# Kernel tuning notes

Measured on AMD Instinct MI355X. Metric: run time of the kernel, lower is better.

Reference implementation:

```python
import jax, jax.numpy as jnp
import numpy as np
import math

IN_FEATURES = 4096
OUT_FEATURES = 4096
NUM_COMPONENTS = 256
TWO_PI = 2.0 * math.pi


def setup_inputs() -> dict:
    key = jax.random.key(0)
    k1, k2, k3, k4 = jax.random.split(key, 4)
    x = jax.random.normal(k1, (4096, IN_FEATURES), dtype=jnp.float32)
    mus = jax.random.uniform(k2, (NUM_COMPONENTS, 2), dtype=jnp.float32)
    log_vars = -3.0 - jax.random.uniform(k3, (NUM_COMPONENTS, 2), dtype=jnp.float32)
    weights = jax.random.uniform(k4, (NUM_COMPONENTS,), dtype=jnp.float32) / NUM_COMPONENTS
    return {"x": x, "mus": mus, "log_vars": log_vars, "weights": weights}


def reference(x, mus, log_vars, weights):
    in_features = x.shape[1]
    x_in_idx = jnp.linspace(0.0, 1.0, in_features, dtype=jnp.float32)    # [I]
    x_out_idx = jnp.linspace(0.0, 1.0, OUT_FEATURES, dtype=jnp.float32)  # [O]
    vars_ = jnp.exp(log_vars)  # [M, 2]

    # Input-side Gaussian basis, fused with 1/sqrt(2*pi*var) and component weight: [I, M]
    d_in = (x_in_idx[:, None] - mus[None, :, 0]) ** 2
    G_in = jnp.exp(-d_in / (2.0 * vars_[None, :, 0])) / jnp.sqrt(TWO_PI * vars_[None, :, 0]) * weights[None, :]
    C = x @ G_in  # [B, M]

    # Output-side Gaussian pdf (Normal(mu1, sigma1).log_prob(x_out).exp()): [M, O]
    d_out = (x_out_idx[None, :] - mus[:, 1:2]) ** 2
    G_out = jnp.exp(-d_out / (2.0 * vars_[:, 1:2])) / jnp.sqrt(TWO_PI * vars_[:, 1:2])

    x_out = (C @ G_out) / (in_features * jnp.sum(weights))  # [B, O]
    return x_out
```

## Files before the change

### kernel.cpp

```cpp
#include <hip/hip_runtime.h>
#include <hip/hip_bf16.h>
#include <math.h>

#define IN_FEAT 4096
#define OUT_FEAT 4096
#define NCOMP 256
#define BATCH 4096
#define TWO_PI_F 6.28318530717958647692f

typedef __attribute__((ext_vector_type(8))) short short8;
typedef __attribute__((ext_vector_type(8))) __bf16 bf16x8;
typedef __attribute__((ext_vector_type(4))) float f32x4;
typedef __attribute__((ext_vector_type(16))) float f32x16;

__device__ __forceinline__ ushort f2b(float f) {
  union { float f; unsigned u; } v; v.f = f;
  unsigned r = (v.u + 0x7fffu + ((v.u >> 16) & 1u)) >> 16;
  return (ushort)r;
}

__device__ __forceinline__ float b2f(short s) {
  union { unsigned u; float f; } v; v.u = ((unsigned)(ushort)s) << 16;
  return v.f;
}

__device__ __forceinline__ bf16x8 ld_frag(const void* p) {
  short8 s = *(const short8*)p;
  return __builtin_bit_cast(bf16x8, s);
}

__device__ __forceinline__ bf16x8 cvt8f(float4 a, float4 b) {
  bf16x8 r;
  r[0] = (__bf16)a.x; r[1] = (__bf16)a.y; r[2] = (__bf16)a.z; r[3] = (__bf16)a.w;
  r[4] = (__bf16)b.x; r[5] = (__bf16)b.y; r[6] = (__bf16)b.z; r[7] = (__bf16)b.w;
  return r;
}

__device__ __forceinline__ void gload_lds16(const void* g, void* l) {
  __builtin_amdgcn_global_load_lds(
      (const __attribute__((address_space(1))) void*)g,
      (__attribute__((address_space(3))) void*)l, 16, 0, 0);
}

__global__ __launch_bounds__(256) void prep_kernel(
    const float* __restrict__ mus, const float* __restrict__ lvs,
    const float* __restrict__ w,
    ushort* __restrict__ Gt, ushort* __restrict__ GoT) {
  int idx = blockIdx.x * 256 + threadIdx.x;
  if (idx < NCOMP * IN_FEAT) {
    int m = idx >> 12, i = idx & (IN_FEAT - 1);
    float v = expf(lvs[2 * m]);
    float d = (float)i * (1.0f / (IN_FEAT - 1)) - mus[2 * m];
    float g = expf(-d * d * (0.5f / v)) * rsqrtf(TWO_PI_F * v) * w[m];
    Gt[idx] = f2b(g);
  } else {
    idx -= NCOMP * IN_FEAT;
    int o = idx >> 8, m = idx & (NCOMP - 1);
    float v = expf(lvs[2 * m + 1]);
    float d = (float)o * (1.0f / (OUT_FEAT - 1)) - mus[2 * m + 1];
    float g = expf(-d * d * (0.5f / v)) * rsqrtf(TWO_PI_F * v);
    GoT[idx] = f2b(g);
  }
}

template<int NS>
__global__ __launch_bounds__(256, 2) void gemm1_kernel(
    const float* __restrict__ x, const ushort* __restrict__ Gt,
    ushort* __restrict__ Cpart) {
  constexpr int KR = IN_FEAT / NS;
  constexpr int NT = KR / 32;
  __shared__ __align__(16) char lds[3 * 24576];
  const int tid = threadIdx.x, wid = tid >> 6, lane = tid & 63;
  const int m0 = blockIdx.x * 128;
  const int n0 = blockIdx.y * 128;
  const int kb0 = blockIdx.z * KR;
  const int l15 = lane & 15, q = lane >> 4;
  const int wr = (wid >> 1) * 64, wc = (wid & 1) * 64;

  f32x4 acc[4][4] = {};

  const int ar = lane >> 3;
  const int aslot = (lane & 7) ^ ar;
  const float* gpa[4];
  #pragma unroll
  for (int i = 0; i < 4; ++i) {
    int c = wid * 4 + i;
    gpa[i] = &x[(size_t)(m0 + c * 8 + ar) * IN_FEAT + kb0 + aslot * 4];
  }
  const int br = lane >> 2;
  const int bsw = (((lane & 3) ^ ((lane >> 3) & 3)) << 3);
  const ushort* gpb[2];
  #pragma unroll
  for (int i = 0; i < 2; ++i) {
    int c = wid * 2 + i;
    gpb[i] = &Gt[(size_t)(n0 + c * 16 + br) * IN_FEAT + kb0 + bsw];
  }
  const int fswz = (q << 4) ^ (((l15 >> 1) & 3) << 4);
  const int akey = l15 & 7;

  #define STAGE(wb_, krel) {                                                 \
    char* Ld = lds + (wb_) * 24576;                                          \
    _Pragma("unroll")                                                        \
    for (int i = 0; i < 4; ++i)                                              \
      gload_lds16(gpa[i] + (krel), Ld + (wid * 4 + i) * 1024 + lane * 16);   \
    _Pragma("unroll")                                                        \
    for (int i = 0; i < 2; ++i)                                              \
      gload_lds16(gpb[i] + (krel),                                           \
                  Ld + 16384 + (wid * 2 + i) * 1024 + lane * 16);            \
  }

  #define COMPUTE(rb_) {                                                     \
    const char* Ab = lds + (rb_) * 24576;                                    \
    const char* Bb = Ab + 16384;                                             \
    bf16x8 bfr[4];                                                           \
    _Pragma("unroll")                                                        \
    for (int nj = 0; nj < 4; ++nj)                                           \
      bfr[nj] = ld_frag(Bb + (wc + nj * 16 + l15) * 64 + fswz);              \
    _Pragma("unroll")                                                        \
    for (int mi = 0; mi < 4; ++mi) {                                         \
      int mr = wr + mi * 16 + l15;                                           \
      float4 f0 = *(const float4*)(Ab + mr * 128 + (((2 * q + 0) ^ akey) << 4)); \
      float4 f1 = *(const float4*)(Ab + mr * 128 + (((2 * q + 1) ^ akey) << 4)); \
      bf16x8 af = cvt8f(f0, f1);                                             \
      _Pragma("unroll")                                                      \
      for (int nj = 0; nj < 4; ++nj)                                         \
        acc[mi][nj] = __builtin_amdgcn_mfma_f32_16x16x32_bf16(af, bfr[nj],   \
                                                   acc[mi][nj], 0, 0, 0);    \
    } }

  #define WAITBAR(n)                                                         \
    asm volatile("s_waitcnt vmcnt(" #n ")" ::: "memory");                    \
    __builtin_amdgcn_s_barrier();                                            \
    __builtin_amdgcn_sched_barrier(0);

  STAGE(0, 0)
  STAGE(1, 32)

  int rb = 0, wb = 2;
  for (int t = 0; t < NT - 2; ++t) {
    WAITBAR(6)
    STAGE(wb, (t + 2) * 32)
    COMPUTE(rb)
    rb = (rb == 2) ? 0 : rb + 1;
    wb = (wb == 2) ? 0 : wb + 1;
  }
  WAITBAR(6)
  COMPUTE(rb)
  rb = (rb == 2) ? 0 : rb + 1;
  WAITBAR(0)
  COMPUTE(rb)

  #undef STAGE
  #undef COMPUTE
  #undef WAITBAR

  ushort* Cp = Cpart + (size_t)blockIdx.z * ((size_t)BATCH * NCOMP);
  #pragma unroll
  for (int mi = 0; mi < 4; ++mi)
    #pragma unroll
    for (int nj = 0; nj < 4; ++nj)
      #pragma unroll
      for (int r = 0; r < 4; ++r) {
        int row = m0 + wr + mi * 16 + q * 4 + r;
        int col = n0 + wc + nj * 16 + l15;
        Cp[(size_t)row * NCOMP + col] = f2b(acc[mi][nj][r]);
      }
}

template<int NS>
__global__ __launch_bounds__(256) void reduce_kernel(ushort* __restrict__ Cp) {
  size_t i = ((size_t)blockIdx.x * 256 + threadIdx.x) * 8;
  float s[8] = {};
  #pragma unroll
  for (int p = 0; p < NS; ++p) {
    short8 v = *(const short8*)&Cp[(size_t)p * BATCH * NCOMP + i];
    #pragma unroll
    for (int e = 0; e < 8; ++e) s[e] += b2f(v[e]);
  }
  short8 hh;
  #pragma unroll
  for (int e = 0; e < 8; ++e) hh[e] = (short)f2b(s[e]);
  *(short8*)&Cp[i] = hh;
}

__global__ __launch_bounds__(256, 4) void gemm2_kernel(
    const ushort* __restrict__ Cb, const ushort* __restrict__ GoT,
    const float* __restrict__ w, float* __restrict__ out) {
  __shared__ __align__(16) ushort lds[2 * 8192];
  const int tid = threadIdx.x, wid = tid >> 6, lane = tid & 63;
  const int m0 = blockIdx.y * 128, n0 = blockIdx.x * 128;
  const int wr = (wid >> 1) * 64, wc = (wid & 1) * 64;
  const int r32 = lane & 31, h = lane >> 5;

  float4 wv = *(const float4*)&w[lane * 4];
  float s = wv.x + wv.y + wv.z + wv.w;
  #pragma unroll
  for (int off = 32; off > 0; off >>= 1) s += __shfl_xor(s, off);
  const float scale = 1.0f / ((float)IN_FEAT * s);

  const int brow = lane >> 2;
  const int bswz = (((lane & 3) ^ ((lane >> 3) & 3)) << 3);
  const int sw0 = (h << 4) ^ (((r32 >> 1) & 3) << 4);

  f32x16 acc[2][2] = {};

  #define STAGE2(buf, k0)                                                    \
    _Pragma("unroll")                                                        \
    for (int q2 = 0; q2 < 2; ++q2) {                                         \
      int c = wid * 2 + q2;                                                  \
      int row = c * 16 + brow;                                               \
      gload_lds16(&Cb[(size_t)(m0 + row) * NCOMP + (k0) + bswz],             \
                  &lds[(buf) * 8192 + c * 512]);                             \
      gload_lds16(&GoT[(size_t)(n0 + row) * NCOMP + (k0) + bswz],            \
                  &lds[(buf) * 8192 + 4096 + c * 512]);                      \
    }

  STAGE2(0, 0)
  __syncthreads();

  for (int t = 0; t < 8; ++t) {
    if (t < 7) STAGE2((t + 1) & 1, (t + 1) * 32)
    const char* base = (const char*)lds + (t & 1) * 16384;
    const char* Bb = base + 8192;
    #pragma unroll
    for (int s2 = 0; s2 < 2; ++s2) {
      const int off = sw0 ^ (s2 << 5);
      bf16x8 a0 = ld_frag(base + (wr + r32) * 64 + off);
      bf16x8 a1 = ld_frag(base + (wr + 32 + r32) * 64 + off);
      bf16x8 b0 = ld_frag(Bb + (wc + r32) * 64 + off);
      bf16x8 b1 = ld_frag(Bb + (wc + 32 + r32) * 64 + off);
      acc[0][0] = __builtin_amdgcn_mfma_f32_32x32x16_bf16(a0, b0, acc[0][0], 0, 0, 0);
      acc[0][1] = __builtin_amdgcn_mfma_f32_32x32x16_bf16(a0, b1, acc[0][1], 0, 0, 0);
      acc[1][0] = __builtin_amdgcn_mfma_f32_32x32x16_bf16(a1, b0, acc[1][0], 0, 0, 0);
      acc[1][1] = __builtin_amdgcn_mfma_f32_32x32x16_bf16(a1, b1, acc[1][1], 0, 0, 0);
    }
    __syncthreads();
  }
  #undef STAGE2

  #pragma unroll
  for (int mi = 0; mi < 2; ++mi)
    #pragma unroll
    for (int nj = 0; nj < 2; ++nj)
      #pragma unroll
      for (int g = 0; g < 16; ++g) {
        int row = m0 + wr + mi * 32 + (g & 3) + 8 * (g >> 2) + 4 * h;
        int col = n0 + wc + nj * 32 + r32;
        out[(size_t)row * OUT_FEAT + col] = acc[mi][nj][g] * scale;
      }
}

extern "C" void kernel_launch(void* const* d_in, const int* in_sizes, int n_in,
                              void* d_out, int out_size, void* d_ws, size_t ws_size,
                              hipStream_t stream) {
  const float* x   = (const float*)d_in[0];
  const float* mus = (const float*)d_in[1];
  const float* lvs = (const float*)d_in[2];
  const float* w   = (const float*)d_in[3];
  float* out = (float*)d_out;

  ushort* Gt  = (ushort*)d_ws;
  ushort* GoT = Gt  + (size_t)NCOMP * IN_FEAT;
  ushort* Cpart = GoT + (size_t)OUT_FEAT * NCOMP;

  const size_t MiB = 1024 * 1024;
  int nsplit = 8;
  while (nsplit > 1 && ws_size < 4 * MiB + (size_t)nsplit * 2 * MiB) nsplit >>= 1;

  prep_kernel<<<(NCOMP * IN_FEAT + OUT_FEAT * NCOMP) / 256, 256, 0, stream>>>(
      mus, lvs, w, Gt, GoT);

  switch (nsplit) {
    case 8:
      gemm1_kernel<8><<<dim3(BATCH / 128, 2, 8), 256, 0, stream>>>(x, Gt, Cpart);
      reduce_kernel<8><<<BATCH * NCOMP / 8 / 256, 256, 0, stream>>>(Cpart);
      break;
    case 4:
      gemm1_kernel<4><<<dim3(BATCH / 128, 2, 4), 256, 0, stream>>>(x, Gt, Cpart);
      reduce_kernel<4><<<BATCH * NCOMP / 8 / 256, 256, 0, stream>>>(Cpart);
      break;
    case 2:
      gemm1_kernel<2><<<dim3(BATCH / 128, 2, 2), 256, 0, stream>>>(x, Gt, Cpart);
      reduce_kernel<2><<<BATCH * NCOMP / 8 / 256, 256, 0, stream>>>(Cpart);
      break;
    default:
      gemm1_kernel<1><<<dim3(BATCH / 128, 2, 1), 256, 0, stream>>>(x, Gt, Cpart);
      break;
  }

  gemm2_kernel<<<dim3(OUT_FEAT / 128, BATCH / 128), 256, 0, stream>>>(
      Cpart, GoT, w, out);
}
```

Measured before the change: 58.06 us.

## Replace LDS-staged gemm1 with direct-global per-wave 16x256 tiles

Rewrites the first GEMM so each wave computes a 16-row by 256-column strip, reading x and Gt fragments straight from global memory into registers instead of staging them through triple-buffered LDS with async loads and barriers. The grid drops the N split, so each x row tile is read once per K split rather than twice. This removes LDS traffic and synchronisation but gives up the LDS pipelining, and the Gt fragment loads become uncoalesced, cached global reads repeated by every wave.

New measurement: 117.7 us. +102.7%, slower.

```diff
diff --git a/kernel.cpp b/kernel.cpp
--- a/kernel.cpp
+++ b/kernel.cpp
@@ -69,102 +69,38 @@
     ushort* __restrict__ Cpart) {
   constexpr int KR = IN_FEAT / NS;
   constexpr int NT = KR / 32;
-  __shared__ __align__(16) char lds[3 * 24576];
   const int tid = threadIdx.x, wid = tid >> 6, lane = tid & 63;
-  const int m0 = blockIdx.x * 128;
-  const int n0 = blockIdx.y * 128;
-  const int kb0 = blockIdx.z * KR;
   const int l15 = lane & 15, q = lane >> 4;
-  const int wr = (wid >> 1) * 64, wc = (wid & 1) * 64;
-
-  f32x4 acc[4][4] = {};
-
-  const int ar = lane >> 3;
-  const int aslot = (lane & 7) ^ ar;
-  const float* gpa[4];
-  #pragma unroll
-  for (int i = 0; i < 4; ++i) {
-    int c = wid * 4 + i;
-    gpa[i] = &x[(size_t)(m0 + c * 8 + ar) * IN_FEAT + kb0 + aslot * 4];
-  }
-  const int br = lane >> 2;
-  const int bsw = (((lane & 3) ^ ((lane >> 3) & 3)) << 3);
-  const ushort* gpb[2];
-  #pragma unroll
-  for (int i = 0; i < 2; ++i) {
-    int c = wid * 2 + i;
-    gpb[i] = &Gt[(size_t)(n0 + c * 16 + br) * IN_FEAT + kb0 + bsw];
-  }
-  const int fswz = (q << 4) ^ (((l15 >> 1) & 3) << 4);
-  const int akey = l15 & 7;
-
-  #define STAGE(wb_, krel) {                                                 \
-    char* Ld = lds + (wb_) * 24576;                                          \
-    _Pragma("unroll")                                                        \
-    for (int i = 0; i < 4; ++i)                                              \
-      gload_lds16(gpa[i] + (krel), Ld + (wid * 4 + i) * 1024 + lane * 16);   \
-    _Pragma("unroll")                                                        \
-    for (int i = 0; i < 2; ++i)                                              \
-      gload_lds16(gpb[i] + (krel),                                           \
-                  Ld + 16384 + (wid * 2 + i) * 1024 + lane * 16);            \
-  }
-
-  #define COMPUTE(rb_) {                                                     \
-    const char* Ab = lds + (rb_) * 24576;                                    \
-    const char* Bb = Ab + 16384;                                             \
-    bf16x8 bfr[4];                                                           \
-    _Pragma("unroll")                                                        \
-    for (int nj = 0; nj < 4; ++nj)                                           \
-      bfr[nj] = ld_frag(Bb + (wc + nj * 16 + l15) * 64 + fswz);              \
-    _Pragma("unroll")                                                        \
-    for (int mi = 0; mi < 4; ++mi) {                                         \
-      int mr = wr + mi * 16 + l15;                                           \
-      float4 f0 = *(const float4*)(Ab + mr * 128 + (((2 * q + 0) ^ akey) << 4)); \
-      float4 f1 = *(const float4*)(Ab + mr * 128 + (((2 * q + 1) ^ akey) << 4)); \
-      bf16x8 af = cvt8f(f0, f1);                                             \
-      _Pragma("unroll")                                                      \
-      for (int nj = 0; nj < 4; ++nj)                                         \
-        acc[mi][nj] = __builtin_amdgcn_mfma_f32_16x16x32_bf16(af, bfr[nj],   \
-                                                   acc[mi][nj], 0, 0, 0);    \
-    } }
-
-  #define WAITBAR(n)                                                         \
-    asm volatile("s_waitcnt vmcnt(" #n ")" ::: "memory");                    \
-    __builtin_amdgcn_s_barrier();                                            \
-    __builtin_amdgcn_sched_barrier(0);
-
-  STAGE(0, 0)
-  STAGE(1, 32)
-
-  int rb = 0, wb = 2;
-  for (int t = 0; t < NT - 2; ++t) {
-    WAITBAR(6)
-    STAGE(wb, (t + 2) * 32)
-    COMPUTE(rb)
-    rb = (rb == 2) ? 0 : rb + 1;
-    wb = (wb == 2) ? 0 : wb + 1;
-  }
-  WAITBAR(6)
-  COMPUTE(rb)
-  rb = (rb == 2) ? 0 : rb + 1;
-  WAITBAR(0)
-  COMPUTE(rb)
-
-  #undef STAGE
-  #undef COMPUTE
-  #undef WAITBAR
-
-  ushort* Cp = Cpart + (size_t)blockIdx.z * ((size_t)BATCH * NCOMP);
-  #pragma unroll
-  for (int mi = 0; mi < 4; ++mi)
-    #pragma unroll
-    for (int nj = 0; nj < 4; ++nj)
-      #pragma unroll
-      for (int r = 0; r < 4; ++r) {
-        int row = m0 + wr + mi * 16 + q * 4 + r;
-        int col = n0 + wc + nj * 16 + l15;
-        Cp[(size_t)row * NCOMP + col] = f2b(acc[mi][nj][r]);
-      }
+  const int m0 = blockIdx.x * 64 + wid * 16;
+  const int kb0 = blockIdx.y * KR;
+
+  f32x4 acc[16] = {};
+
+  const float*  xp = &x[(size_t)(m0 + l15) * IN_FEAT + kb0 + q * 8];
+  const ushort* gp = &Gt[(size_t)l15 * IN_FEAT + kb0 + q * 8];
+
+  #pragma unroll 2
+  for (int t = 0; t < NT; ++t) {
+    const int k = t * 32;
+    float4 a0 = *(const float4*)(xp + k);
+    float4 a1 = *(const float4*)(xp + k + 4);
+    bf16x8 af = cvt8f(a0, a1);
+    #pragma unroll
+    for (int nf = 0; nf < 16; ++nf) {
+      bf16x8 bf = ld_frag(gp + (size_t)nf * 16 * IN_FEAT + k);
+      acc[nf] = __builtin_amdgcn_mfma_f32_16x16x32_bf16(af, bf, acc[nf], 0, 0, 0);
+    }
+  }
+
+  ushort* Cp = Cpart + (size_t)blockIdx.y * ((size_t)BATCH * NCOMP);
+  #pragma unroll
+  for (int nf = 0; nf < 16; ++nf)
+    #pragma unroll
+    for (int r = 0; r < 4; ++r) {
+      int row = m0 + q * 4 + r;
+      int col = nf * 16 + l15;
+      Cp[(size_t)row * NCOMP + col] = f2b(acc[nf][r]);
+    }
 }
 
 template<int NS>
@@ -272,19 +208,19 @@
 
   switch (nsplit) {
     case 8:
-      gemm1_kernel<8><<<dim3(BATCH / 128, 2, 8), 256, 0, stream>>>(x, Gt, Cpart);
+      gemm1_kernel<8><<<dim3(BATCH / 64, 8), 256, 0, stream>>>(x, Gt, Cpart);
       reduce_kernel<8><<<BATCH * NCOMP / 8 / 256, 256, 0, stream>>>(Cpart);
       break;
     case 4:
-      gemm1_kernel<4><<<dim3(BATCH / 128, 2, 4), 256, 0, stream>>>(x, Gt, Cpart);
+      gemm1_kernel<4><<<dim3(BATCH / 64, 4), 256, 0, stream>>>(x, Gt, Cpart);
       reduce_kernel<4><<<BATCH * NCOMP / 8 / 256, 256, 0, stream>>>(Cpart);
       break;
     case 2:
-      gemm1_kernel<2><<<dim3(BATCH / 128, 2, 2), 256, 0, stream>>>(x, Gt, Cpart);
+      gemm1_kernel<2><<<dim3(BATCH / 64, 2), 256, 0, stream>>>(x, Gt, Cpart);
       reduce_kernel<2><<<BATCH * NCOMP / 8 / 256, 256, 0, stream>>>(Cpart);
       break;
     default:
-      gemm1_kernel<1><<<dim3(BATCH / 128, 2, 1), 256, 0, stream>>>(x, Gt, Cpart);
+      gemm1_kernel<1><<<dim3(BATCH / 64, 1), 256, 0, stream>>>(x, Gt, Cpart);
       break;
   }
 
```
